# Optimization experiments

Hardware: AMD Instinct MI355X
Metric: run time of the kernel (lower is better)

Reference implementation:

```python
import jax, jax.numpy as jnp
import numpy as np

B, N, NODE_DIM = 8, 128, 64
L, RES_DIM = 512, 1024
CG, CP = 128, 128
NUM_GNN_STEPS = 3
HID = CG + CP // 2  # interaction hidden = 192


def setup_inputs() -> dict:
    key = jax.random.key(0)
    ks = jax.random.split(key, 20)
    a = (jax.random.uniform(ks[0], (B, N, N)) < 0.05).astype(jnp.float32)
    adj = jnp.clip(a + jnp.swapaxes(a, 1, 2), 0.0, 1.0)
    adj = adj * (1.0 - jnp.eye(N, dtype=jnp.float32))
    nodes = jax.random.normal(ks[1], (B, N, NODE_DIM), dtype=jnp.float32)
    prot = jax.random.normal(ks[2], (B, L, RES_DIM), dtype=jnp.float32)
    s = 0.02
    inp = {
        "adj_mats": adj, "nodes": nodes, "protein_sequences": prot,
        "Wn": jax.random.normal(ks[3], (NODE_DIM, CG)) * s, "bn": jnp.zeros((CG,)),
        "Wg": jax.random.normal(ks[4], (CG, CG)) * s, "bg": jnp.zeros((CG,)),
        "Wr": jax.random.normal(ks[5], (RES_DIM, CP)) * s, "br": jnp.zeros((CP,)),
        "Wa": jax.random.normal(ks[6], (CG + CP, 1)) * s, "ba": jnp.zeros((1,)),
        "W1": jax.random.normal(ks[7], (CG + CP, HID)) * s, "b1": jnp.zeros((HID,)),
        "W2": jax.random.normal(ks[8], (HID, CG)) * s, "b2": jnp.zeros((CG,)),
        "Wo": jax.random.normal(ks[9], (CG, 1)) * s, "bo": jnp.zeros((1,)),
    }
    return inp


def reference(adj_mats, nodes, protein_sequences,
              Wn, bn, Wg, bg, Wr, br, Wa, ba, W1, b1, W2, b2, Wo, bo):
    # node compression: [B,N,CG]
    h = nodes @ Wn + bn
    deg = jnp.clip(jnp.sum(adj_mats, axis=-1), 1.0, None)        # [B,N]
    norm = deg ** -0.5                                           # [B,N]
    for i in range(NUM_GNN_STEPS):
        m = jnp.einsum('bij,bjc->bic', adj_mats, h * norm[..., None])
        h = (m * norm[..., None]) @ Wg + bg
        h = jnp.tanh(h) if i == NUM_GNN_STEPS - 1 else jax.nn.relu(h)
    # residue compression: [B,L,CP]
    r = protein_sequences @ Wr + br
    # MergeSnE1: all-pairs broadcast concat -> [B, N*L, CG+CP]
    cat = jnp.concatenate([
        jnp.broadcast_to(h[:, :, None, :], (B, N, L, CG)),
        jnp.broadcast_to(r[:, None, :, :], (B, N, L, CP)),
    ], axis=-1).reshape(B, N * L, CG + CP)
    # attention: Linear -> Softmax over last dim (size 1 => all ones, faithful)
    attn = jax.nn.softmax(cat @ Wa + ba, axis=-1)                # [B,N*L,1]
    inter = jax.nn.relu(cat @ W1 + b1) @ W2 + b2                 # [B,N*L,CG]
    weighted_sum = jnp.sum(attn * inter, axis=1)                 # [B,CG]
    return weighted_sum @ Wo + bo                                # [B,1]
```

## Files before the change

kernel.cpp:

```cpp
#include <hip/hip_runtime.h>

#define BB 8
#define NN 128
#define ND 64
#define LL 512
#define RD 1024
#define CG 128
#define HID 192

typedef __attribute__((ext_vector_type(8))) short short8;
typedef __attribute__((ext_vector_type(4))) float f32x4;

__device__ __forceinline__ unsigned short f2bf(float x) {
    unsigned u = __builtin_bit_cast(unsigned, x);
    u += 0x7fffu + ((u >> 16) & 1u);
    return (unsigned short)(u >> 16);
}
__device__ __forceinline__ float bf2f(unsigned short h) {
    unsigned u = ((unsigned)h) << 16;
    return __builtin_bit_cast(float, u);
}
#define MFMA __builtin_amdgcn_mfma_f32_16x16x32_bf16

__global__ __launch_bounds__(512, 1) void k_prep(
    const float* __restrict__ adj, const float* __restrict__ nodes,
    const float* __restrict__ Wn, const float* __restrict__ bn,
    const float* __restrict__ Wr, const float* __restrict__ br,
    const float* __restrict__ W1, const float* __restrict__ b1,
    const float* __restrict__ Wg, const float* __restrict__ bg,
    const float* __restrict__ W2, const float* __restrict__ b2,
    const float* __restrict__ Wo, const float* __restrict__ bo,
    unsigned short* __restrict__ WcT, float* __restrict__ hW1T,
    float* __restrict__ vbuf, float* __restrict__ cconst,
    float* __restrict__ acc, unsigned* __restrict__ ctr)
{
    __shared__ unsigned short hT[NN][136];
    __shared__ unsigned short mbuf[NN][72];
    __shared__ unsigned short WgT[NN][136];
    __shared__ unsigned short W1T[HID][136];
    __shared__ float snorm[NN];
    __shared__ float b1cL[HID];
    __shared__ float sbg[NN];
    int t = threadIdx.x, blk = blockIdx.x;
    const float* W1b = W1 + CG * HID;

    if (blk < 64) {
        int r0 = blk * 16;
        float* sW = (float*)&hT[0][0];
        for (int e = t; e < 16 * CG; e += 512) sW[e] = Wr[(size_t)r0 * CG + e];
        __syncthreads();
        for (int o = t; o < 16 * HID; o += 512) {
            int r = o / HID, c = o % HID;
            float s = 0.f;
            #pragma unroll 8
            for (int m = 0; m < CG; ++m)
                s = fmaf(sW[r * CG + m], W1b[(size_t)m * HID + c], s);
            WcT[(size_t)c * RD + r0 + r] = f2bf(s);
        }
        return;
    }
    if (blk == 64) {
        if (t < HID) {
            float s = 0.f;
            #pragma unroll 8
            for (int k = 0; k < CG; ++k) s = fmaf(W2[t * CG + k], Wo[k], s);
            vbuf[t] = s;
        }
        if (t == 511) {
            float s = 0.f;
            for (int k = 0; k < CG; ++k) s = fmaf(b2[k], Wo[k], s);
            cconst[0] = (float)(NN * LL) * s + bo[0];
        }
        if (t == 510) *ctr = 0u;
        if (t < BB) acc[t] = 0.f;
        return;
    }

    int b = blk - 65;
    int w = t >> 6, l = t & 63, lr = l & 15, ks = l >> 4, lk = ks * 8;
    int i0 = w * 16;

    {
        float* dscr = (float*)&mbuf[0][0];
        int row = t >> 2, q4 = t & 3;
        const float* ar = adj + ((size_t)b * NN + row) * NN + q4 * 32;
        float d = 0.f;
        #pragma unroll
        for (int c4 = 0; c4 < 8; ++c4) {
            float4 p = *(const float4*)(ar + c4 * 4);
            d += (p.x + p.y) + (p.z + p.w);
        }
        dscr[row * 4 + q4] = d;
        __syncthreads();
        if (t < NN) {
            snorm[t] = rsqrtf(fmaxf(dscr[t*4] + dscr[t*4+1] + dscr[t*4+2] + dscr[t*4+3], 1.f));
        } else if (t < 320) {
            int j = t - 128;
            float s = b1[j];
            #pragma unroll 8
            for (int m = 0; m < CG; ++m)
                s = fmaf(br[m], W1b[(size_t)m * HID + j], s);
            b1cL[j] = s;
        } else if (t < 448) {
            sbg[t - 320] = bg[t - 320];
        }
        __syncthreads();
    }

    unsigned short* WnT = &mbuf[0][0];
    #pragma unroll
    for (int q = 0; q < 16; ++q) {
        int e = t + 512 * q;
        int c = e & 127, k = e >> 7;
        WnT[c * 72 + k] = f2bf(Wn[(size_t)k * CG + c]);
    }
    #pragma unroll
    for (int q = 0; q < 32; ++q) {
        int e = t + 512 * q;
        int c = e & 127, j = e >> 7;
        WgT[c][j] = f2bf(Wg[(size_t)j * CG + c]);
    }
    #pragma unroll
    for (int q = 0; q < 32; ++q) {
        int e = t + 512 * q;
        int jj = e & 127, k = e >> 7;
        W1T[jj][k] = f2bf(W1[(size_t)k * HID + jj]);
    }
    #pragma unroll
    for (int q = 0; q < 16; ++q) {
        int e = t + 512 * q;
        int jj = 128 + (e & 63), k = e >> 6;
        W1T[jj][k] = f2bf(W1[(size_t)k * HID + jj]);
    }

    short8 af[4];
    {
        float ni = snorm[i0 + lr];
        const float* ar = adj + ((size_t)b * NN + i0 + lr) * NN;
        #pragma unroll
        for (int kk = 0; kk < 4; ++kk) {
            int kb = kk * 32 + lk;
            float4 p0 = *(const float4*)(ar + kb);
            float4 p1 = *(const float4*)(ar + kb + 4);
            unsigned short u[8];
            u[0] = f2bf(p0.x * ni * snorm[kb+0]); u[1] = f2bf(p0.y * ni * snorm[kb+1]);
            u[2] = f2bf(p0.z * ni * snorm[kb+2]); u[3] = f2bf(p0.w * ni * snorm[kb+3]);
            u[4] = f2bf(p1.x * ni * snorm[kb+4]); u[5] = f2bf(p1.y * ni * snorm[kb+5]);
            u[6] = f2bf(p1.z * ni * snorm[kb+6]); u[7] = f2bf(p1.w * ni * snorm[kb+7]);
            af[kk] = *(const short8*)u;
        }
    }
    short8 bnod[2];
    #pragma unroll
    for (int kk = 0; kk < 2; ++kk) {
        const float* np = nodes + ((size_t)b * NN + i0 + lr) * ND + kk * 32 + lk;
        float4 q0 = *(const float4*)np;
        float4 q1 = *(const float4*)(np + 4);
        unsigned short u[8];
        u[0]=f2bf(q0.x); u[1]=f2bf(q0.y); u[2]=f2bf(q0.z); u[3]=f2bf(q0.w);
        u[4]=f2bf(q1.x); u[5]=f2bf(q1.y); u[6]=f2bf(q1.z); u[7]=f2bf(q1.w);
        bnod[kk] = *(const short8*)u;
    }
    __syncthreads();

    #pragma unroll
    for (int ct = 0; ct < 8; ++ct) {
        f32x4 d = {0.f, 0.f, 0.f, 0.f};
        #pragma unroll
        for (int kk = 0; kk < 2; ++kk) {
            short8 afw = *(const short8*)(WnT + (ct * 16 + lr) * 72 + kk * 32 + lk);
            d = MFMA(afw, bnod[kk], d, 0, 0, 0);
        }
        #pragma unroll
        for (int i = 0; i < 4; ++i)
            hT[ct * 16 + ks * 4 + i][i0 + lr] = f2bf(d[i] + bn[ct * 16 + ks * 4 + i]);
    }
    __syncthreads();

    for (int s = 0; s < 3; ++s) {
        f32x4 acc8[8];
        #pragma unroll
        for (int ct = 0; ct < 8; ++ct) acc8[ct] = (f32x4){0.f, 0.f, 0.f, 0.f};
        #pragma unroll
        for (int hf = 0; hf < 2; ++hf) {
            #pragma unroll
            for (int jt = 0; jt < 4; ++jt) {
                int jg = hf * 64 + jt * 16;
                f32x4 d = {0.f, 0.f, 0.f, 0.f};
                #pragma unroll
                for (int kk = 0; kk < 4; ++kk) {
                    short8 bf = *(const short8*)(&hT[jg + lr][kk * 32 + lk]);
                    d = MFMA(af[kk], bf, d, 0, 0, 0);
                }
                #pragma unroll
                for (int i = 0; i < 4; ++i)
                    mbuf[i0 + ks * 4 + i][jt * 16 + lr] = f2bf(d[i]);
            }
            short8 bm[2];
            #pragma unroll
            for (int kk = 0; kk < 2; ++kk)
                bm[kk] = *(const short8*)(&mbuf[i0 + lr][kk * 32 + lk]);
            #pragma unroll
            for (int ct = 0; ct < 8; ++ct) {
                #pragma unroll
                for (int kk = 0; kk < 2; ++kk) {
                    short8 wf = *(const short8*)(&WgT[ct * 16 + lr][hf * 64 + kk * 32 + lk]);
                    if (s < 2)
                        acc8[ct] = MFMA(wf, bm[kk], acc8[ct], 0, 0, 0);
                    else
                        acc8[ct] = MFMA(bm[kk], wf, acc8[ct], 0, 0, 0);
                }
            }
        }
        __syncthreads();
        if (s < 2) {
            #pragma unroll
            for (int ct = 0; ct < 8; ++ct)
                #pragma unroll
                for (int i = 0; i < 4; ++i)
                    hT[ct * 16 + ks * 4 + i][i0 + lr] =
                        f2bf(fmaxf(acc8[ct][i] + sbg[ct * 16 + ks * 4 + i], 0.f));
        } else {
            #pragma unroll
            for (int ct = 0; ct < 8; ++ct)
                #pragma unroll
                for (int i = 0; i < 4; ++i)
                    hT[i0 + ks * 4 + i][ct * 16 + lr] =
                        f2bf(tanhf(acc8[ct][i] + sbg[ct * 16 + lr]));
        }
        __syncthreads();
    }

    {
        short8 bh[4];
        #pragma unroll
        for (int kk = 0; kk < 4; ++kk)
            bh[kk] = *(const short8*)(&hT[i0 + lr][kk * 32 + lk]);
        #pragma unroll
        for (int jjt = 0; jjt < 12; ++jjt) {
            f32x4 d = {0.f, 0.f, 0.f, 0.f};
            #pragma unroll
            for (int kk = 0; kk < 4; ++kk) {
                short8 wf = *(const short8*)(&W1T[jjt * 16 + lr][kk * 32 + lk]);
                d = MFMA(wf, bh[kk], d, 0, 0, 0);
            }
            #pragma unroll
            for (int i = 0; i < 4; ++i) {
                int jj = jjt * 16 + ks * 4 + i;
                hW1T[(size_t)b * HID * NN + jj * NN + i0 + lr] = d[i] + b1cL[jj];
            }
        }
    }
}

__global__ __launch_bounds__(512, 1) void k_gemm(
    const float* __restrict__ prot, const unsigned short* __restrict__ WcT,
    const float* __restrict__ hW1T, const float* __restrict__ vbuf,
    float* __restrict__ acc, const float* __restrict__ cconst,
    unsigned* __restrict__ ctr, float* __restrict__ out)
{
    __shared__ char ubuf[57600];
    unsigned short* aT = (unsigned short*)ubuf;
    float* pbuf = (float*)(ubuf + 33024);
    unsigned short* h1 = (unsigned short*)ubuf;
    __shared__ float sred[8];
    __shared__ int lastf;
    int t = threadIdx.x, blk = blockIdx.x;
    int b = blk >> 5, lc = blk & 31;
    int w = t >> 6, l = t & 63, lr = l & 15, ks = l >> 4, lk = ks * 8;
    int w2 = w >> 2, wj = w & 3;

    {
        int row = t >> 5, seg = t & 31;
        const float* pr = prot + ((size_t)(b * LL + lc * 16 + row)) * RD + seg * 32;
        unsigned short* dst = aT + row * 1032 + seg * 32;
        #pragma unroll
        for (int c8 = 0; c8 < 4; ++c8) {
            float4 p0 = *(const float4*)(pr + c8 * 8);
            float4 p1 = *(const float4*)(pr + c8 * 8 + 4);
            unsigned short u[8];
            u[0]=f2bf(p0.x); u[1]=f2bf(p0.y); u[2]=f2bf(p0.z); u[3]=f2bf(p0.w);
            u[4]=f2bf(p1.x); u[5]=f2bf(p1.y); u[6]=f2bf(p1.z); u[7]=f2bf(p1.w);
            *(short8*)(dst + c8 * 8) = *(const short8*)u;
        }
    }
    __syncthreads();

    f32x4 a0 = {0.f,0.f,0.f,0.f}, a1 = a0, a2 = a0;
    {
        const unsigned short* ap = aT + lr * 1032 + w2 * 512 + lk;
        const unsigned short* bp = WcT + (size_t)(wj * 48 + lr) * RD + w2 * 512 + lk;
        #pragma unroll 4
        for (int k0 = 0; k0 < 512; k0 += 32) {
            short8 av = *(const short8*)(ap + k0);
            short8 b0 = *(const short8*)(bp + k0);
            short8 b1 = *(const short8*)(bp + 16 * RD + k0);
            short8 b2 = *(const short8*)(bp + 32 * RD + k0);
            a0 = MFMA(av, b0, a0, 0, 0, 0);
            a1 = MFMA(av, b1, a1, 0, 0, 0);
            a2 = MFMA(av, b2, a2, 0, 0, 0);
        }
    }
    #pragma unroll
    for (int i = 0; i < 4; ++i) {
        int r = ks * 4 + i;
        pbuf[(w2 * 16 + r) * 192 + wj * 48 + lr]      = a0[i];
        pbuf[(w2 * 16 + r) * 192 + wj * 48 + 16 + lr] = a1[i];
        pbuf[(w2 * 16 + r) * 192 + wj * 48 + 32 + lr] = a2[i];
    }
    __syncthreads();
    float rw0[4], rw1[4], rw2[4];
    #pragma unroll
    for (int i = 0; i < 4; ++i) {
        int r = ks * 4 + i;
        rw0[i] = pbuf[r * 192 + wj*48 + lr]      + pbuf[(16 + r) * 192 + wj*48 + lr];
        rw1[i] = pbuf[r * 192 + wj*48 + 16 + lr] + pbuf[(16 + r) * 192 + wj*48 + 16 + lr];
        rw2[i] = pbuf[r * 192 + wj*48 + 32 + lr] + pbuf[(16 + r) * 192 + wj*48 + 32 + lr];
    }
    __syncthreads();

    for (int e = t; e < HID * NN; e += 512) {
        int row = e >> 7, n = e & 127;
        h1[row * 136 + n] = f2bf(hW1T[(size_t)b * HID * NN + e]);
    }
    __syncthreads();

    float v0 = vbuf[wj * 48 + lr];
    float v1 = vbuf[wj * 48 + 16 + lr];
    float v2 = vbuf[wj * 48 + 32 + lr];
    const unsigned short* h0p = h1 + (wj * 48 + lr) * 136 + w2 * 64;
    const unsigned short* h1p = h0p + 16 * 136;
    const unsigned short* h2p = h0p + 32 * 136;
    float s = 0.f;
    #pragma unroll 2
    for (int n0 = 0; n0 < 64; n0 += 4) {
        unsigned short e0[4], e1[4], e2[4];
        *(uint2*)e0 = *(const uint2*)(h0p + n0);
        *(uint2*)e1 = *(const uint2*)(h1p + n0);
        *(uint2*)e2 = *(const uint2*)(h2p + n0);
        #pragma unroll
        for (int q = 0; q < 4; ++q) {
            float hh0 = bf2f(e0[q]), hh1 = bf2f(e1[q]), hh2 = bf2f(e2[q]);
            #pragma unroll
            for (int i = 0; i < 4; ++i) {
                s = fmaf(v0, fmaxf(rw0[i] + hh0, 0.f), s);
                s = fmaf(v1, fmaxf(rw1[i] + hh1, 0.f), s);
                s = fmaf(v2, fmaxf(rw2[i] + hh2, 0.f), s);
            }
        }
    }
    for (int off = 32; off; off >>= 1) s += __shfl_down(s, off);
    if (l == 0) sred[w] = s;
    __syncthreads();
    if (t == 0) {
        float tot = ((sred[0] + sred[1]) + (sred[2] + sred[3]))
                  + ((sred[4] + sred[5]) + (sred[6] + sred[7]));
        atomicAdd(&acc[b], tot);
        __threadfence();
        unsigned old = atomicAdd(ctr, 1u);
        lastf = (old == gridDim.x - 1) ? 1 : 0;
    }
    __syncthreads();
    if (lastf && t < BB)
        out[t] = atomicAdd(&acc[t], 0.0f) + cconst[0];
}

extern "C" void kernel_launch(void* const* d_in, const int* in_sizes, int n_in,
                              void* d_out, int out_size, void* d_ws, size_t ws_size,
                              hipStream_t stream)
{
    const float* adj   = (const float*)d_in[0];
    const float* nodes = (const float*)d_in[1];
    const float* prot  = (const float*)d_in[2];
    const float* Wn    = (const float*)d_in[3];
    const float* bn    = (const float*)d_in[4];
    const float* Wg    = (const float*)d_in[5];
    const float* bg    = (const float*)d_in[6];
    const float* Wr    = (const float*)d_in[7];
    const float* br    = (const float*)d_in[8];
    const float* W1    = (const float*)d_in[11];
    const float* b1    = (const float*)d_in[12];
    const float* W2    = (const float*)d_in[13];
    const float* b2    = (const float*)d_in[14];
    const float* Wo    = (const float*)d_in[15];
    const float* bo    = (const float*)d_in[16];

    float* ws     = (float*)d_ws;
    float* hW1T   = ws;
    float* vbuf   = ws + 196608;
    float* cconst = ws + 196800;
    float* accb   = ws + 196804;
    unsigned* ctr = (unsigned*)(ws + 196812);
    unsigned short* WcT = (unsigned short*)(ws + 196816);
    float* out    = (float*)d_out;

    hipLaunchKernelGGL(k_prep, dim3(73), dim3(512), 0, stream,
                       adj, nodes, Wn, bn, Wr, br, W1, b1, Wg, bg,
                       W2, b2, Wo, bo, WcT, hW1T, vbuf, cconst, accb, ctr);
    hipLaunchKernelGGL(k_gemm, dim3(256), dim3(512), 0, stream,
                       prot, WcT, hW1T, vbuf, accb, cconst, ctr, out);
}
```

Measured before the change: 61.13 us.

## Use MFMA for Wr·W1 fold, preload h1 early, atomically accumulate into output

The prep kernel now computes the folded Wr·W1b weight product with bf16 MFMA tiles over 16 blocks, replacing the scalar FMA loop spread over 64 blocks. The GEMM kernel loads the per-batch hW1T table into its own shared buffer alongside the protein tile, so one barrier pass drops out. The last-block counter and finalize step are removed: the prep kernel writes the constant term to the output and each GEMM block atomically adds its partial sum. This uses more shared memory and adds bf16 rounding to the folded weight computation.

```diff
diff --git a/kernel.cpp b/kernel.cpp
--- a/kernel.cpp
+++ b/kernel.cpp
@@ -31,8 +31,7 @@
     const float* __restrict__ W2, const float* __restrict__ b2,
     const float* __restrict__ Wo, const float* __restrict__ bo,
     unsigned short* __restrict__ WcT, float* __restrict__ hW1T,
-    float* __restrict__ vbuf, float* __restrict__ cconst,
-    float* __restrict__ acc, unsigned* __restrict__ ctr)
+    float* __restrict__ vbuf, float* __restrict__ out)
 {
     __shared__ unsigned short hT[NN][136];
     __shared__ unsigned short mbuf[NN][72];
@@ -42,42 +41,62 @@
     __shared__ float b1cL[HID];
     __shared__ float sbg[NN];
     int t = threadIdx.x, blk = blockIdx.x;
+    int w = t >> 6, l = t & 63, lr = l & 15, ks = l >> 4, lk = ks * 8;
     const float* W1b = W1 + CG * HID;
 
-    if (blk < 64) {
-        int r0 = blk * 16;
-        float* sW = (float*)&hT[0][0];
-        for (int e = t; e < 16 * CG; e += 512) sW[e] = Wr[(size_t)r0 * CG + e];
+    if (blk < 16) {
+        int r0 = blk * 64;
+        #pragma unroll
+        for (int q = 0; q < 48; ++q) {
+            int e = t + 512 * q;
+            int m = e / HID, c = e % HID;
+            W1T[c][m] = f2bf(W1[(size_t)(CG + m) * HID + c]);
+        }
+        int rt = w & 3, jh = w >> 2;
+        short8 awr[4];
+        #pragma unroll
+        for (int kk = 0; kk < 4; ++kk) {
+            const float* wp = Wr + (size_t)(r0 + rt * 16 + lr) * CG + kk * 32 + lk;
+            float4 q0 = *(const float4*)wp;
+            float4 q1 = *(const float4*)(wp + 4);
+            unsigned short u[8];
+            u[0]=f2bf(q0.x); u[1]=f2bf(q0.y); u[2]=f2bf(q0.z); u[3]=f2bf(q0.w);
+            u[4]=f2bf(q1.x); u[5]=f2bf(q1.y); u[6]=f2bf(q1.z); u[7]=f2bf(q1.w);
+            awr[kk] = *(const short8*)u;
+        }
         __syncthreads();
-        for (int o = t; o < 16 * HID; o += 512) {
-            int r = o / HID, c = o % HID;
-            float s = 0.f;
-            #pragma unroll 8
-            for (int m = 0; m < CG; ++m)
-                s = fmaf(sW[r * CG + m], W1b[(size_t)m * HID + c], s);
-            WcT[(size_t)c * RD + r0 + r] = f2bf(s);
+        #pragma unroll
+        for (int jt6 = 0; jt6 < 6; ++jt6) {
+            int jt = jh * 6 + jt6;
+            f32x4 d = {0.f, 0.f, 0.f, 0.f};
+            #pragma unroll
+            for (int kk = 0; kk < 4; ++kk) {
+                short8 bf = *(const short8*)(&W1T[jt * 16 + lr][kk * 32 + lk]);
+                d = MFMA(awr[kk], bf, d, 0, 0, 0);
+            }
+            unsigned short u[4];
+            #pragma unroll
+            for (int i = 0; i < 4; ++i) u[i] = f2bf(d[i]);
+            *(uint2*)(WcT + (size_t)(jt * 16 + lr) * RD + r0 + rt * 16 + ks * 4) = *(uint2*)u;
         }
         return;
     }
-    if (blk == 64) {
+    if (blk == 16) {
         if (t < HID) {
             float s = 0.f;
             #pragma unroll 8
             for (int k = 0; k < CG; ++k) s = fmaf(W2[t * CG + k], Wo[k], s);
             vbuf[t] = s;
         }
-        if (t == 511) {
+        if (t < BB) {
             float s = 0.f;
             for (int k = 0; k < CG; ++k) s = fmaf(b2[k], Wo[k], s);
-            cconst[0] = (float)(NN * LL) * s + bo[0];
-        }
-        if (t == 510) *ctr = 0u;
-        if (t < BB) acc[t] = 0.f;
+            out[t] = (float)(NN * LL) * s + bo[0];
+        }
         return;
     }
 
-    int b = blk - 65;
-    int w = t >> 6, l = t & 63, lr = l & 15, ks = l >> 4, lk = ks * 8;
+    int b = blk - 17;
     int i0 = w * 16;
 
     {
@@ -256,15 +275,12 @@
 __global__ __launch_bounds__(512, 1) void k_gemm(
     const float* __restrict__ prot, const unsigned short* __restrict__ WcT,
     const float* __restrict__ hW1T, const float* __restrict__ vbuf,
-    float* __restrict__ acc, const float* __restrict__ cconst,
-    unsigned* __restrict__ ctr, float* __restrict__ out)
+    float* __restrict__ out)
 {
-    __shared__ char ubuf[57600];
-    unsigned short* aT = (unsigned short*)ubuf;
-    float* pbuf = (float*)(ubuf + 33024);
-    unsigned short* h1 = (unsigned short*)ubuf;
+    __shared__ unsigned short aT[16 * 1032];
+    __shared__ unsigned short h1[HID * 136];
+    __shared__ float pbuf[2 * 16 * 192];
     __shared__ float sred[8];
-    __shared__ int lastf;
     int t = threadIdx.x, blk = blockIdx.x;
     int b = blk >> 5, lc = blk & 31;
     int w = t >> 6, l = t & 63, lr = l & 15, ks = l >> 4, lk = ks * 8;
@@ -284,6 +300,15 @@
             *(short8*)(dst + c8 * 8) = *(const short8*)u;
         }
     }
+    #pragma unroll
+    for (int q = 0; q < 48; ++q) {
+        int e = t + 512 * q;
+        int row = e >> 7, n = e & 127;
+        h1[row * 136 + n] = f2bf(hW1T[(size_t)b * HID * NN + e]);
+    }
+    float v0 = vbuf[wj * 48 + lr];
+    float v1 = vbuf[wj * 48 + 16 + lr];
+    float v2 = vbuf[wj * 48 + 32 + lr];
     __syncthreads();
 
     f32x4 a0 = {0.f,0.f,0.f,0.f}, a1 = a0, a2 = a0;
@@ -317,17 +342,7 @@
         rw1[i] = pbuf[r * 192 + wj*48 + 16 + lr] + pbuf[(16 + r) * 192 + wj*48 + 16 + lr];
         rw2[i] = pbuf[r * 192 + wj*48 + 32 + lr] + pbuf[(16 + r) * 192 + wj*48 + 32 + lr];
     }
-    __syncthreads();
-
-    for (int e = t; e < HID * NN; e += 512) {
-        int row = e >> 7, n = e & 127;
-        h1[row * 136 + n] = f2bf(hW1T[(size_t)b * HID * NN + e]);
-    }
-    __syncthreads();
-
-    float v0 = vbuf[wj * 48 + lr];
-    float v1 = vbuf[wj * 48 + 16 + lr];
-    float v2 = vbuf[wj * 48 + 32 + lr];
+
     const unsigned short* h0p = h1 + (wj * 48 + lr) * 136 + w2 * 64;
     const unsigned short* h1p = h0p + 16 * 136;
     const unsigned short* h2p = h0p + 32 * 136;
@@ -355,14 +370,8 @@
     if (t == 0) {
         float tot = ((sred[0] + sred[1]) + (sred[2] + sred[3]))
                   + ((sred[4] + sred[5]) + (sred[6] + sred[7]));
-        atomicAdd(&acc[b], tot);
-        __threadfence();
-        unsigned old = atomicAdd(ctr, 1u);
-        lastf = (old == gridDim.x - 1) ? 1 : 0;
-    }
-    __syncthreads();
-    if (lastf && t < BB)
-        out[t] = atomicAdd(&acc[t], 0.0f) + cconst[0];
+        atomicAdd(&out[b], tot);
+    }
 }
 
 extern "C" void kernel_launch(void* const* d_in, const int* in_sizes, int n_in,
@@ -388,15 +397,12 @@
     float* ws     = (float*)d_ws;
     float* hW1T   = ws;
     float* vbuf   = ws + 196608;
-    float* cconst = ws + 196800;
-    float* accb   = ws + 196804;
-    unsigned* ctr = (unsigned*)(ws + 196812);
-    unsigned short* WcT = (unsigned short*)(ws + 196816);
+    unsigned short* WcT = (unsigned short*)(ws + 196800);
     float* out    = (float*)d_out;
 
-    hipLaunchKernelGGL(k_prep, dim3(73), dim3(512), 0, stream,
+    hipLaunchKernelGGL(k_prep, dim3(25), dim3(512), 0, stream,
                        adj, nodes, Wn, bn, Wr, br, W1, b1, Wg, bg,
-                       W2, b2, Wo, bo, WcT, hW1T, vbuf, cconst, accb, ctr);
+                       W2, b2, Wo, bo, WcT, hW1T, vbuf, out);
     hipLaunchKernelGGL(k_gemm, dim3(256), dim3(512), 0, stream,
-                       prot, WcT, hW1T, vbuf, accb, cconst, ctr, out);
+                       prot, WcT, hW1T, vbuf, out);
 }
```

Measured after the change: 56.37 us. -7.8%, faster.
